# Kernel tuning notes

Hardware: AMD Instinct MI355X
Metric: run time of the kernel (lower is better)

## Reference

```python
import jax, jax.numpy as jnp
import numpy as np

NEG_INF = -1e30

def _pool_unpool(x, k):
    # x: [B, C, H, W]. Non-overlapping max pool with window k (floor-mode,
    # matching torch MaxPool2d default), then MaxUnpool: scatter the pooled max
    # back to its argmax location within each window, zeros elsewhere.
    B, C, H, W = x.shape
    Hc, Wc = (H // k) * k, (W // k) * k  # cropped region covered by windows
    xc = x[:, :, :Hc, :Wc]
    # reshape into windows: [B, C, H/k, k, W/k, k] -> [B, C, H/k, W/k, k*k]
    xw = xc.reshape(B, C, Hc // k, k, Wc // k, k).transpose(0, 1, 2, 4, 3, 5)
    xw = xw.reshape(B, C, Hc // k, Wc // k, k * k)
    mx = jnp.max(xw, axis=-1, keepdims=True)
    am = jnp.argmax(xw, axis=-1)  # first max index, matches torch tie-breaking
    onehot = (jnp.arange(k * k) == am[..., None])
    yw = jnp.where(onehot, mx, jnp.zeros_like(mx))
    yc = yw.reshape(B, C, Hc // k, Wc // k, k, k).transpose(0, 1, 2, 4, 3, 5)
    yc = yc.reshape(B, C, Hc, Wc)
    # output_size=size in torch unpool -> pad uncovered border with zeros
    return jnp.pad(yc, ((0, 0), (0, 0), (0, H - Hc), (0, W - Wc)))

def setup_inputs() -> dict:
    key = jax.random.key(0)
    x = jax.random.uniform(key, (16, 1, 1080, 1920), dtype=jnp.float32)
    return {"x": x}

def reference(x):
    k = 3
    x = _pool_unpool(x, k)
    x = _pool_unpool(x, k + 2)
    x = _pool_unpool(x, k + 3)
    return x
```

## Files before the change

### kernel.cpp

```cpp
#include <hip/hip_runtime.h>


#define IMG_H 1080
#define IMG_W 1920
#define TILE 30
#define NTHREADS 64

template <int K>
__device__ __forceinline__ void nms_stage(float (*tile)[TILE], int t) {
    constexpr int NW = TILE / K;
    for (int w = t; w < NW * NW; w += NTHREADS) {
        const int wr = w / NW;
        const int wc = w - wr * NW;
        const int r0 = wr * K;
        const int c0 = wc * K;
        float mx = -1.0f;
        int am = 0;
#pragma unroll
        for (int r = 0; r < K; ++r)
#pragma unroll
            for (int c = 0; c < K; ++c) {
                const float v = tile[r0 + r][c0 + c];
                if (v > mx) { mx = v; am = r * K + c; }
            }
#pragma unroll
        for (int r = 0; r < K; ++r)
#pragma unroll
            for (int c = 0; c < K; ++c)
                tile[r0 + r][c0 + c] = (r * K + c == am) ? mx : 0.0f;
    }
    __syncthreads();
}

__global__ __launch_bounds__(NTHREADS) void pooling_nms_kernel(
    const float* __restrict__ x, float* __restrict__ out) {
    __shared__ float tile[TILE][TILE];

    const int t = threadIdx.x;
    const int col0 = blockIdx.x * TILE;
    const int row0 = blockIdx.y * TILE;
    const size_t base = (size_t)blockIdx.z * (IMG_H * (size_t)IMG_W) +
                        (size_t)row0 * IMG_W + col0;
    const float* src = x + base;
    float* dst = out + base;

    constexpr int V2PR = TILE / 2;
    constexpr int NV = TILE * V2PR;
    for (int i = t; i < NV; i += NTHREADS) {
        const int r = i / V2PR;
        const int c2 = i - r * V2PR;
        const float2 v =
            *reinterpret_cast<const float2*>(src + (size_t)r * IMG_W + c2 * 2);
        *reinterpret_cast<float2*>(&tile[r][c2 * 2]) = v;
    }
    __syncthreads();

    nms_stage<3>(tile, t);
    nms_stage<5>(tile, t);
    nms_stage<6>(tile, t);

    for (int i = t; i < NV; i += NTHREADS) {
        const int r = i / V2PR;
        const int c2 = i - r * V2PR;
        *reinterpret_cast<float2*>(dst + (size_t)r * IMG_W + c2 * 2) =
            *reinterpret_cast<const float2*>(&tile[r][c2 * 2]);
    }
}

extern "C" void kernel_launch(void* const* d_in, const int* in_sizes, int n_in,
                              void* d_out, int out_size, void* d_ws, size_t ws_size,
                              hipStream_t stream) {
    const float* x = (const float*)d_in[0];
    float* out = (float*)d_out;
    dim3 grid(IMG_W / TILE, IMG_H / TILE, 16);
    pooling_nms_kernel<<<grid, NTHREADS, 0, stream>>>(x, out);
}
```

Before: 284.1 us.

## Keep tile rows in registers and resolve window maxima with wave shuffles

Drops the shared-memory tile. Each lane now holds one 30-element row of a 30x30 tile in registers, and each wave covers two tiles. Window maxima are found by taking a max within each row and then reducing across the K rows of a window with __shfl, with first-max tie-breaking done through row and column ordering. Blocks grow to 256 threads (4 waves, 8 tiles). The aim is to remove LDS traffic and barriers and to make global accesses wider, at the cost of higher register use and two idle lanes per half-wave.

```diff
diff --git a/kernel.cpp b/kernel.cpp
--- a/kernel.cpp
+++ b/kernel.cpp
@@ -1,69 +1,93 @@
 #include <hip/hip_runtime.h>
+#include <stdint.h>
 
 
 #define IMG_H 1080
 #define IMG_W 1920
-#define TILE 30
-#define NTHREADS 64
 
 template <int K>
-__device__ __forceinline__ void nms_stage(float (*tile)[TILE], int t) {
-    constexpr int NW = TILE / K;
-    for (int w = t; w < NW * NW; w += NTHREADS) {
-        const int wr = w / NW;
-        const int wc = w - wr * NW;
-        const int r0 = wr * K;
-        const int c0 = wc * K;
-        float mx = -1.0f;
-        int am = 0;
+__device__ __forceinline__ void stage(float (&v)[30], int rc, int h) {
+    constexpr int NH = 30 / K;
+    const int g = rc / K;
+    const int myrr = rc - g * K;
+    const int srcbase = (h << 5) + g * K;
 #pragma unroll
-        for (int r = 0; r < K; ++r)
+    for (int j = 0; j < NH; ++j) {
+        float hm = v[j * K];
 #pragma unroll
-            for (int c = 0; c < K; ++c) {
-                const float v = tile[r0 + r][c0 + c];
-                if (v > mx) { mx = v; am = r * K + c; }
-            }
+        for (int c = 1; c < K; ++c) hm = fmaxf(hm, v[j * K + c]);
+        float m = -1.0f;
+        int fr = -1;
 #pragma unroll
-        for (int r = 0; r < K; ++r)
+        for (int rr = 0; rr < K; ++rr) {
+            const float tv = __shfl(hm, srcbase + rr, 64);
+            if (tv > m) { m = tv; fr = rr; }
+        }
+        const bool rowwin = (fr == myrr);
+        bool seen = false;
 #pragma unroll
-            for (int c = 0; c < K; ++c)
-                tile[r0 + r][c0 + c] = (r * K + c == am) ? mx : 0.0f;
+        for (int c = 0; c < K; ++c) {
+            const bool eq = (v[j * K + c] == m);
+            if (!(rowwin && eq && !seen)) v[j * K + c] = 0.0f;
+            seen = seen || eq;
+        }
     }
-    __syncthreads();
 }
 
-__global__ __launch_bounds__(NTHREADS) void pooling_nms_kernel(
+__global__ __launch_bounds__(256) void pooling_nms_kernel(
     const float* __restrict__ x, float* __restrict__ out) {
-    __shared__ float tile[TILE][TILE];
+    const int t = threadIdx.x;
+    const int w = t >> 6;
+    const int lane = t & 63;
+    const int h = lane >> 5;
+    const int r = lane & 31;
+    const int rc = (r < 30) ? r : 29;
 
-    const int t = threadIdx.x;
-    const int col0 = blockIdx.x * TILE;
-    const int row0 = blockIdx.y * TILE;
+    const int col0 = blockIdx.x * 240 + w * 60 + h * 30;
     const size_t base = (size_t)blockIdx.z * (IMG_H * (size_t)IMG_W) +
-                        (size_t)row0 * IMG_W + col0;
+                        (size_t)(blockIdx.y * 30 + rc) * IMG_W + col0;
     const float* src = x + base;
     float* dst = out + base;
 
-    constexpr int V2PR = TILE / 2;
-    constexpr int NV = TILE * V2PR;
-    for (int i = t; i < NV; i += NTHREADS) {
-        const int r = i / V2PR;
-        const int c2 = i - r * V2PR;
-        const float2 v =
-            *reinterpret_cast<const float2*>(src + (size_t)r * IMG_W + c2 * 2);
-        *reinterpret_cast<float2*>(&tile[r][c2 * 2]) = v;
+    float v[30];
+    if (r < 30) {
+        if (h == 0) {
+#pragma unroll
+            for (int q = 0; q < 7; ++q)
+                *reinterpret_cast<float4*>(&v[4 * q]) =
+                    *reinterpret_cast<const float4*>(src + 4 * q);
+            *reinterpret_cast<float2*>(&v[28]) =
+                *reinterpret_cast<const float2*>(src + 28);
+        } else {
+            *reinterpret_cast<float2*>(&v[0]) =
+                *reinterpret_cast<const float2*>(src);
+#pragma unroll
+            for (int q = 0; q < 7; ++q)
+                *reinterpret_cast<float4*>(&v[2 + 4 * q]) =
+                    *reinterpret_cast<const float4*>(src + 2 + 4 * q);
+        }
     }
-    __syncthreads();
 
-    nms_stage<3>(tile, t);
-    nms_stage<5>(tile, t);
-    nms_stage<6>(tile, t);
+    stage<3>(v, rc, h);
+    stage<5>(v, rc, h);
+    stage<6>(v, rc, h);
 
-    for (int i = t; i < NV; i += NTHREADS) {
-        const int r = i / V2PR;
-        const int c2 = i - r * V2PR;
-        *reinterpret_cast<float2*>(dst + (size_t)r * IMG_W + c2 * 2) =
-            *reinterpret_cast<const float2*>(&tile[r][c2 * 2]);
+    if (r < 30) {
+        if (h == 0) {
+#pragma unroll
+            for (int q = 0; q < 7; ++q)
+                *reinterpret_cast<float4*>(dst + 4 * q) =
+                    *reinterpret_cast<const float4*>(&v[4 * q]);
+            *reinterpret_cast<float2*>(dst + 28) =
+                *reinterpret_cast<const float2*>(&v[28]);
+        } else {
+            *reinterpret_cast<float2*>(dst) =
+                *reinterpret_cast<const float2*>(&v[0]);
+#pragma unroll
+            for (int q = 0; q < 7; ++q)
+                *reinterpret_cast<float4*>(dst + 2 + 4 * q) =
+                    *reinterpret_cast<const float4*>(&v[2 + 4 * q]);
+        }
     }
 }
 
@@ -72,6 +96,6 @@
                               hipStream_t stream) {
     const float* x = (const float*)d_in[0];
     float* out = (float*)d_out;
-    dim3 grid(IMG_W / TILE, IMG_H / TILE, 16);
-    pooling_nms_kernel<<<grid, NTHREADS, 0, stream>>>(x, out);
+    dim3 grid(IMG_W / 240, IMG_H / 30, 16);
+    pooling_nms_kernel<<<grid, 256, 0, stream>>>(x, out);
 }
```

Measured after the change: 288.7 us. Within noise of the previous version (+1.6%).
